# Kernel tuning notes

Hardware: AMD Instinct MI355X
Metric: run time of the kernel (lower is better)

Reference implementation:

```python
import jax, jax.numpy as jnp
import numpy as np

B, S, H, HKV, D = 4, 1024, 32, 8, 128   # batch segments, seq per segment, q heads, kv heads, head dim
N = B * S                                # Ntotal (ragged tokens, equal-length segments)
SCALE = 1.0 / np.sqrt(D)                 # softmax_scale init kwarg
NEG = -1e9


def setup_inputs() -> dict:
    key = jax.random.key(0)
    kq, kk, kv = jax.random.split(key, 3)
    q = jax.random.normal(kq, (N, H, D), jnp.float32)
    k = jax.random.normal(kk, (N, HKV, D), jnp.float32)
    v = jax.random.normal(kv, (N, HKV, D), jnp.float32)
    # RoPE angles, rotate-half convention: concat(freqs, freqs), broadcast over heads
    inv_freq = 1.0 / (10000.0 ** (jnp.arange(D // 2, dtype=jnp.float32) / (D // 2)))
    pos = jnp.arange(S, dtype=jnp.float32)
    ang = pos[:, None] * inv_freq[None, :]                      # [S, D/2]
    idx_theta = jnp.tile(jnp.concatenate([ang, ang], -1), (B, 1))[:, None, :]  # [N,1,D]
    # per-segment causal mask, stacked -> [N, S]
    causal = jnp.where(jnp.arange(S)[None, :] <= jnp.arange(S)[:, None], 0.0, NEG).astype(jnp.float32)
    mask = jnp.tile(causal, (B, 1))
    return {"q": q, "k": k, "v": v, "idx_theta": idx_theta, "mask": mask}


def _rotate_half(x):
    # cat(-x[..., D/2:], x[..., :D/2])
    return jnp.concatenate([-x[..., D // 2:], x[..., : D // 2]], axis=-1)


def reference(q, k, v, idx_theta, mask):
    rep = H // HKV
    # repeat_kv: attention head i uses kv head i // rep (matches torch expand+reshape order)
    kx = jnp.repeat(k, rep, axis=1)                    # [N, H, D]
    vx = jnp.repeat(v, rep, axis=1)
    cos, sin = jnp.cos(idx_theta), jnp.sin(idx_theta)
    qr = q * cos + _rotate_half(q) * sin
    kr = kx * cos + _rotate_half(kx) * sin
    # segment-blocked attention (equal-length segments, vectorized over batch & heads)
    qb = qr.reshape(B, S, H, D)
    kb = kr.reshape(B, S, H, D)
    vb = vx.reshape(B, S, H, D)
    mb = mask.reshape(B, S, S)[:, None, :, :]          # [B,1,S,S]
    scores = jnp.einsum('bqhd,bkhd->bhqk', qb, kb) * SCALE + mb
    l = jax.nn.logsumexp(scores, axis=-1)              # [B,H,S] == max + logsumexp(shifted)
    p = jax.nn.softmax(scores, axis=-1)
    o = jnp.einsum('bhqk,bkhd->bqhd', p, vb)           # [B,S,H,D]
    o = o.reshape(N, H * D)                            # o.reshape(Ntotal, num_head, -1) flattened last two in torch is (N,H,D)->(N,H,D); original reshape(q.shape[0], q.shape[1], -1) keeps [N,H,D]
    o = o.reshape(N, H, D)
    l = l.transpose(0, 2, 1).reshape(N, H, 1)          # [Ntotal, num_head, 1]
    return o, l
```

## Files before the change

kernel.cpp:

```cpp
#include <hip/hip_runtime.h>

#define B_    4
#define S_    1024
#define H_    32
#define HKV_  8
#define D_    128
#define NTOT  (B_*S_)
#define QT_   64
#define KT_   32
#define DPAD  (D_+8)
#define KPAD  (KT_+8)

#define SCALE_ 0.08838834764831845f

typedef __attribute__((ext_vector_type(8))) short bf16x8;
typedef __attribute__((ext_vector_type(4))) short bf16x4;
typedef __attribute__((ext_vector_type(4))) float f32x4;
typedef __attribute__((ext_vector_type(4))) int   int4v;

__device__ __forceinline__ unsigned short f2bf(float f) {
    unsigned int u = __float_as_uint(f);
    u += 0x7FFFu + ((u >> 16) & 1u);
    return (unsigned short)(u >> 16);
}
__device__ __forceinline__ unsigned int pack2bf(float a, float b) {
    return (unsigned int)f2bf(a) | ((unsigned int)f2bf(b) << 16);
}

__global__ void rope_k_kernel(const float* __restrict__ k,
                              const float* __restrict__ theta,
                              unsigned short* __restrict__ kr) {
    int t  = blockIdx.x * blockDim.x + threadIdx.x;
    int g  = t & 7;
    int hk = (t >> 3) & (HKV_ - 1);
    int n  = t >> 6;
    if (n >= NTOT) return;
    int d0 = g * 8;
    const float* kp = k + ((size_t)n * HKV_ + hk) * D_;
    const float* tp = theta + (size_t)n * D_;

    alignas(16) float kl[8], ku[8], thl[8], thu[8];
    *(float4*)&kl[0]  = *(const float4*)(kp + d0);
    *(float4*)&kl[4]  = *(const float4*)(kp + d0 + 4);
    *(float4*)&ku[0]  = *(const float4*)(kp + d0 + 64);
    *(float4*)&ku[4]  = *(const float4*)(kp + d0 + 68);
    *(float4*)&thl[0] = *(const float4*)(tp + d0);
    *(float4*)&thl[4] = *(const float4*)(tp + d0 + 4);
    *(float4*)&thu[0] = *(const float4*)(tp + d0 + 64);
    *(float4*)&thu[4] = *(const float4*)(tp + d0 + 68);

    alignas(16) unsigned short ol[8], ou[8];
#pragma unroll
    for (int j = 0; j < 8; ++j) {
        float sl, cl, su, cu;
        __sincosf(thl[j], &sl, &cl);
        __sincosf(thu[j], &su, &cu);
        ol[j] = f2bf(kl[j] * cl - ku[j] * sl);
        ou[j] = f2bf(ku[j] * cu + kl[j] * su);
    }
    unsigned short* outp = kr + ((size_t)n * HKV_ + hk) * D_;
    *(int4v*)(outp + d0)      = *(const int4v*)ol;
    *(int4v*)(outp + d0 + 64) = *(const int4v*)ou;
}

__global__ void vt_kernel(const float* __restrict__ v,
                          unsigned short* __restrict__ vt) {
    __shared__ unsigned int T[64][64];
    int blk = blockIdx.x;
    int s0  = (blk & (S_/64 - 1)) * 64;
    int hk  = (blk >> 4) & (HKV_ - 1);
    int b   = blk >> 7;
    int tid = threadIdx.x;

#pragma unroll
    for (int i = 0; i < 8; ++i) {
        int u  = tid + 256 * i;
        int s  = u >> 5;
        int G  = u & 31;
        float4 val = *(const float4*)(v + (((size_t)(b * S_ + s0 + s)) * HKV_ + hk) * D_ + G * 4);
        unsigned int* p = &T[s][(G ^ (s & 31)) << 1];
        p[0] = pack2bf(val.x, val.y);
        p[1] = pack2bf(val.z, val.w);
    }
    __syncthreads();
#pragma unroll
    for (int i = 0; i < 4; ++i) {
        int u = tid + 256 * i;
        int d = u >> 3;
        int g = u & 7;
        int G = d >> 2;
        int half = (d >> 1) & 1;
        int hi   = (d & 1) * 16;
        alignas(16) unsigned short tmp[8];
#pragma unroll
        for (int j = 0; j < 8; ++j) {
            int s = g * 8 + j;
            unsigned int w = T[s][(((G ^ (s & 31)) << 1)) + half];
            tmp[j] = (unsigned short)(w >> hi);
        }
        *(int4v*)(vt + (((size_t)(b * HKV_ + hk)) * D_ + d) * S_ + s0 + g * 8) = *(const int4v*)tmp;
    }
}

__global__ __launch_bounds__(256, 4)
void flash_kernel(const float* __restrict__ q,
                  const float* __restrict__ theta,
                  const unsigned short* __restrict__ kr,
                  const unsigned short* __restrict__ vt,
                  float* __restrict__ o_out,
                  float* __restrict__ l_out) {
    __shared__ unsigned short Ks[2][KT_][DPAD];
    __shared__ unsigned short Vs[2][D_][KPAD];

    const int tid  = threadIdx.x;
    const int wave = tid >> 6;
    const int lane = tid & 63;
    const int l16  = lane & 15;
    const int quad = lane >> 4;

    const int bh = blockIdx.x;
    const int b  = bh >> 5;
    const int h  = bh & (H_ - 1);
    const int hk = h >> 2;
    const int qt = (S_/QT_ - 1) - blockIdx.y;
    const int qbase = qt * QT_;
    const int wq   = qbase + wave * 16;
    const int qrow = wq + l16;

    bf16x8 qfrag[4];
    {
        const int n = b * S_ + qrow;
        const float* qp = q + ((size_t)n * H_ + h) * D_;
        const float* tp = theta + (size_t)n * D_;
#pragma unroll
        for (int c = 0; c < 4; ++c) {
            const int d0 = c * 32 + quad * 8;
            const int dp = d0 ^ 64;
            alignas(16) float qa[8], qb[8], th[8];
            *(float4*)&qa[0] = *(const float4*)(qp + d0);
            *(float4*)&qa[4] = *(const float4*)(qp + d0 + 4);
            *(float4*)&qb[0] = *(const float4*)(qp + dp);
            *(float4*)&qb[4] = *(const float4*)(qp + dp + 4);
            *(float4*)&th[0] = *(const float4*)(tp + d0);
            *(float4*)&th[4] = *(const float4*)(tp + d0 + 4);
            alignas(16) unsigned short tmp[8];
#pragma unroll
            for (int j = 0; j < 8; ++j) {
                float sv, cv;
                __sincosf(th[j], &sv, &cv);
                float rot = (d0 < 64) ? -qb[j] : qb[j];
                tmp[j] = f2bf((qa[j] * cv + rot * sv) * SCALE_);
            }
            qfrag[c] = *(const bf16x8*)tmp;
        }
    }

    f32x4 acc[8];
#pragma unroll
    for (int dt = 0; dt < 8; ++dt) acc[dt] = (f32x4){0.f, 0.f, 0.f, 0.f};
    float m_st = -1e30f, l_st = 0.f;

    const unsigned short* kseg = kr + ((size_t)b * S_ * HKV_ + hk) * D_;
    const unsigned short* vseg = vt + ((size_t)(b * HKV_ + hk)) * D_ * S_;

    const int ku0 = tid, ku1 = tid + 256;
    const int kk0 = ku0 >> 4, kg0 = (ku0 & 15) * 8;
    const int kk1 = kk0 + 16,  kg1 = kg0;
    const int vd0 = tid >> 2, vg0 = (tid & 3) * 8;
    const int vd1 = vd0 + 64,  vg1 = vg0;
    int4v pK0, pK1, pV0, pV1;

#define LOAD_TILE(K0)                                                          \
    do {                                                                       \
        pK0 = *(const int4v*)(kseg + (size_t)((K0) + kk0) * (HKV_*D_) + kg0);  \
        pK1 = *(const int4v*)(kseg + (size_t)((K0) + kk1) * (HKV_*D_) + kg1);  \
        pV0 = *(const int4v*)(vseg + (size_t)vd0 * S_ + (K0) + vg0);           \
        pV1 = *(const int4v*)(vseg + (size_t)vd1 * S_ + (K0) + vg1);           \
    } while (0)
#define STORE_TILE(BUF)                                                        \
    do {                                                                       \
        *(int4v*)&Ks[BUF][kk0][kg0] = pK0;                                     \
        *(int4v*)&Ks[BUF][kk1][kg1] = pK1;                                     \
        *(int4v*)&Vs[BUF][vd0][vg0] = pV0;                                     \
        *(int4v*)&Vs[BUF][vd1][vg1] = pV1;                                     \
    } while (0)

    const int n_kt = 2 * (qt + 1);
    LOAD_TILE(0);
    STORE_TILE(0);

    for (int kt = 0; kt < n_kt; ++kt) {
        const int k0 = kt * KT_;
        const int buf = kt & 1;
        __syncthreads();
        if (kt + 1 < n_kt) LOAD_TILE(k0 + KT_);

        int dd = wq + 15 - k0;
        int nact = dd < 0 ? 0 : (dd >> 4) + 1;
        if (nact > 2) nact = 2;

        if (nact > 0) {
            f32x4 sc[2];
#pragma unroll
            for (int kc = 0; kc < 2; ++kc) {
                if (kc < nact) {
                    f32x4 c = (f32x4){0.f, 0.f, 0.f, 0.f};
#pragma unroll
                    for (int cc = 0; cc < 4; ++cc) {
                        bf16x8 kf = *(const bf16x8*)&Ks[buf][kc * 16 + l16][cc * 32 + quad * 8];
                        c = __builtin_amdgcn_mfma_f32_16x16x32_bf16(kf, qfrag[cc], c, 0, 0, 0);
                    }
                    sc[kc] = c;
                }
            }

            float s[8];
#pragma unroll
            for (int kc = 0; kc < 2; ++kc)
#pragma unroll
                for (int r = 0; r < 4; ++r) {
                    int key = k0 + kc * 16 + quad * 4 + r;
                    s[kc * 4 + r] = (kc < nact && key <= qrow) ? sc[kc][r] : -1e30f;
                }
            float tmax = s[0];
#pragma unroll
            for (int i = 1; i < 8; ++i) tmax = fmaxf(tmax, s[i]);
            tmax = fmaxf(tmax, __shfl_xor(tmax, 16));
            tmax = fmaxf(tmax, __shfl_xor(tmax, 32));
            float mnew  = fmaxf(m_st, tmax);
            float alpha = __expf(m_st - mnew);

            unsigned int pk[4];
            float rs = 0.f;
#pragma unroll
            for (int kc = 0; kc < 2; ++kc) {
                float p0 = __expf(s[kc * 4 + 0] - mnew);
                float p1 = __expf(s[kc * 4 + 1] - mnew);
                float p2 = __expf(s[kc * 4 + 2] - mnew);
                float p3 = __expf(s[kc * 4 + 3] - mnew);
                rs += (p0 + p1) + (p2 + p3);
                pk[kc * 2 + 0] = pack2bf(p0, p1);
                pk[kc * 2 + 1] = pack2bf(p2, p3);
            }
            rs += __shfl_xor(rs, 16);
            rs += __shfl_xor(rs, 32);
            l_st = l_st * alpha + rs;
            m_st = mnew;
#pragma unroll
            for (int dt = 0; dt < 8; ++dt) {
                acc[dt][0] *= alpha; acc[dt][1] *= alpha;
                acc[dt][2] *= alpha; acc[dt][3] *= alpha;
            }

#pragma unroll
            for (int kc = 0; kc < 2; ++kc) {
                if (kc < nact) {
                    union { unsigned int u[2]; bf16x4 v; } pb;
                    pb.u[0] = pk[kc * 2 + 0];
                    pb.u[1] = pk[kc * 2 + 1];
#if __has_builtin(__builtin_amdgcn_mfma_f32_16x16x16bf16_1k)
#pragma unroll
                    for (int dt = 0; dt < 8; ++dt) {
                        bf16x4 vf = *(const bf16x4*)&Vs[buf][dt * 16 + l16][kc * 16 + quad * 4];
                        acc[dt] = __builtin_amdgcn_mfma_f32_16x16x16bf16_1k(vf, pb.v, acc[dt], 0, 0, 0);
                    }
#else
                    bf16x8 pb8 = (bf16x8){pb.v[0], pb.v[1], pb.v[2], pb.v[3], 0, 0, 0, 0};
#pragma unroll
                    for (int dt = 0; dt < 8; ++dt) {
                        bf16x4 vf = *(const bf16x4*)&Vs[buf][dt * 16 + l16][kc * 16 + quad * 4];
                        bf16x8 vf8 = (bf16x8){vf[0], vf[1], vf[2], vf[3], 0, 0, 0, 0};
                        acc[dt] = __builtin_amdgcn_mfma_f32_16x16x32_bf16(vf8, pb8, acc[dt], 0, 0, 0);
                    }
#endif
                }
            }
        }

        if (kt + 1 < n_kt) STORE_TILE(1 - buf);
    }

    const float inv = 1.0f / l_st;
    const int n = b * S_ + qrow;
    float* op = o_out + ((size_t)n * H_ + h) * D_;
#pragma unroll
    for (int dt = 0; dt < 8; ++dt) {
        float4 o4 = {acc[dt][0] * inv, acc[dt][1] * inv, acc[dt][2] * inv, acc[dt][3] * inv};
        *(float4*)(op + dt * 16 + quad * 4) = o4;
    }
    if (quad == 0)
        l_out[(size_t)n * H_ + h] = m_st + logf(l_st);
}

extern "C" void kernel_launch(void* const* d_in, const int* in_sizes, int n_in,
                              void* d_out, int out_size, void* d_ws, size_t ws_size,
                              hipStream_t stream) {
    const float* q     = (const float*)d_in[0];
    const float* k     = (const float*)d_in[1];
    const float* v     = (const float*)d_in[2];
    const float* theta = (const float*)d_in[3];

    float* o_out = (float*)d_out;
    float* l_out = o_out + (size_t)NTOT * H_ * D_;

    unsigned short* kr = (unsigned short*)d_ws;
    unsigned short* vt = kr + (size_t)NTOT * HKV_ * D_;

    rope_k_kernel<<<(NTOT * HKV_ * 8) / 256, 256, 0, stream>>>(k, theta, kr);
    vt_kernel<<<B_ * HKV_ * (S_ / 64), 256, 0, stream>>>(v, vt);

    dim3 grid(B_ * H_, S_ / QT_);
    flash_kernel<<<grid, 256, 0, stream>>>(q, theta, kr, vt, o_out, l_out);
}
```

Baseline: 228.2 us.

## Share K/V tiles across GQA heads per block, use exp2 and lazy rescale

Each block now handles one KV head, and its four waves each take one of the four query heads that share it. Every wave processes two 16-row query groups over a 32-row query tile, so each K/V tile loaded into shared memory is reused across the whole GQA group instead of being reloaded per query head. Softmax switches to base-2 exponentials, with log2e folded into the Q scale. The rescale of the running max and accumulators is skipped when no lane's max grows. V padding changes to 36 with split 8-byte stores, and register pressure roughly doubles (two accumulator sets), so launch bounds drop to 3 blocks per CU. The grid shrinks from 128×16 to 32×32 blocks.

```diff
diff --git a/kernel.cpp b/kernel.cpp
--- a/kernel.cpp
+++ b/kernel.cpp
@@ -6,17 +6,20 @@
 #define HKV_  8
 #define D_    128
 #define NTOT  (B_*S_)
-#define QT_   64
+#define QT_   32
 #define KT_   32
 #define DPAD  (D_+8)
-#define KPAD  (KT_+8)
-
-#define SCALE_ 0.08838834764831845f
+#define VPAD  36
+
+#define SCALE_  0.08838834764831845f
+#define LOG2E_  1.4426950408889634f
+#define LN2_    0.6931471805599453f
 
 typedef __attribute__((ext_vector_type(8))) short bf16x8;
 typedef __attribute__((ext_vector_type(4))) short bf16x4;
 typedef __attribute__((ext_vector_type(4))) float f32x4;
 typedef __attribute__((ext_vector_type(4))) int   int4v;
+typedef __attribute__((ext_vector_type(2))) int   int2v;
 
 __device__ __forceinline__ unsigned short f2bf(float f) {
     unsigned int u = __float_as_uint(f);
@@ -102,7 +105,7 @@
     }
 }
 
-__global__ __launch_bounds__(256, 4)
+__global__ __launch_bounds__(256, 3)
 void flash_kernel(const float* __restrict__ q,
                   const float* __restrict__ theta,
                   const unsigned short* __restrict__ kr,
@@ -110,7 +113,7 @@
                   float* __restrict__ o_out,
                   float* __restrict__ l_out) {
     __shared__ unsigned short Ks[2][KT_][DPAD];
-    __shared__ unsigned short Vs[2][D_][KPAD];
+    __shared__ unsigned short Vs[2][D_][VPAD];
 
     const int tid  = threadIdx.x;
     const int wave = tid >> 6;
@@ -118,17 +121,17 @@
     const int l16  = lane & 15;
     const int quad = lane >> 4;
 
-    const int bh = blockIdx.x;
-    const int b  = bh >> 5;
-    const int h  = bh & (H_ - 1);
-    const int hk = h >> 2;
-    const int qt = (S_/QT_ - 1) - blockIdx.y;
+    const int bkv = blockIdx.x;
+    const int b   = bkv >> 3;
+    const int hkv = bkv & 7;
+    const int h   = hkv * 4 + wave;
+    const int qt  = (S_/QT_ - 1) - blockIdx.y;
     const int qbase = qt * QT_;
-    const int wq   = qbase + wave * 16;
-    const int qrow = wq + l16;
-
-    bf16x8 qfrag[4];
-    {
+
+    bf16x8 qfrag[2][4];
+#pragma unroll
+    for (int mg = 0; mg < 2; ++mg) {
+        const int qrow = qbase + mg * 16 + l16;
         const int n = b * S_ + qrow;
         const float* qp = q + ((size_t)n * H_ + h) * D_;
         const float* tp = theta + (size_t)n * D_;
@@ -149,43 +152,47 @@
                 float sv, cv;
                 __sincosf(th[j], &sv, &cv);
                 float rot = (d0 < 64) ? -qb[j] : qb[j];
-                tmp[j] = f2bf((qa[j] * cv + rot * sv) * SCALE_);
-            }
-            qfrag[c] = *(const bf16x8*)tmp;
+                tmp[j] = f2bf((qa[j] * cv + rot * sv) * (SCALE_ * LOG2E_));
+            }
+            qfrag[mg][c] = *(const bf16x8*)tmp;
         }
     }
 
-    f32x4 acc[8];
-#pragma unroll
-    for (int dt = 0; dt < 8; ++dt) acc[dt] = (f32x4){0.f, 0.f, 0.f, 0.f};
-    float m_st = -1e30f, l_st = 0.f;
-
-    const unsigned short* kseg = kr + ((size_t)b * S_ * HKV_ + hk) * D_;
-    const unsigned short* vseg = vt + ((size_t)(b * HKV_ + hk)) * D_ * S_;
-
-    const int ku0 = tid, ku1 = tid + 256;
-    const int kk0 = ku0 >> 4, kg0 = (ku0 & 15) * 8;
-    const int kk1 = kk0 + 16,  kg1 = kg0;
+    f32x4 acc[2][8];
+#pragma unroll
+    for (int mg = 0; mg < 2; ++mg)
+#pragma unroll
+        for (int dt = 0; dt < 8; ++dt) acc[mg][dt] = (f32x4){0.f, 0.f, 0.f, 0.f};
+    float m_st[2] = {-1e30f, -1e30f};
+    float l_st[2] = {0.f, 0.f};
+
+    const unsigned short* kseg = kr + ((size_t)b * S_ * HKV_ + hkv) * D_;
+    const unsigned short* vseg = vt + ((size_t)(b * HKV_ + hkv)) * D_ * S_;
+
+    const int kk0 = tid >> 4, kg0 = (tid & 15) * 8;
+    const int kk1 = kk0 + 16;
     const int vd0 = tid >> 2, vg0 = (tid & 3) * 8;
-    const int vd1 = vd0 + 64,  vg1 = vg0;
+    const int vd1 = vd0 + 64;
     int4v pK0, pK1, pV0, pV1;
 
 #define LOAD_TILE(K0)                                                          \
     do {                                                                       \
         pK0 = *(const int4v*)(kseg + (size_t)((K0) + kk0) * (HKV_*D_) + kg0);  \
-        pK1 = *(const int4v*)(kseg + (size_t)((K0) + kk1) * (HKV_*D_) + kg1);  \
+        pK1 = *(const int4v*)(kseg + (size_t)((K0) + kk1) * (HKV_*D_) + kg0);  \
         pV0 = *(const int4v*)(vseg + (size_t)vd0 * S_ + (K0) + vg0);           \
-        pV1 = *(const int4v*)(vseg + (size_t)vd1 * S_ + (K0) + vg1);           \
+        pV1 = *(const int4v*)(vseg + (size_t)vd1 * S_ + (K0) + vg0);           \
     } while (0)
 #define STORE_TILE(BUF)                                                        \
     do {                                                                       \
         *(int4v*)&Ks[BUF][kk0][kg0] = pK0;                                     \
-        *(int4v*)&Ks[BUF][kk1][kg1] = pK1;                                     \
-        *(int4v*)&Vs[BUF][vd0][vg0] = pV0;                                     \
-        *(int4v*)&Vs[BUF][vd1][vg1] = pV1;                                     \
+        *(int4v*)&Ks[BUF][kk1][kg0] = pK1;                                     \
+        *(int2v*)&Vs[BUF][vd0][vg0]     = (int2v){pV0.x, pV0.y};               \
+        *(int2v*)&Vs[BUF][vd0][vg0 + 4] = (int2v){pV0.z, pV0.w};               \
+        *(int2v*)&Vs[BUF][vd1][vg0]     = (int2v){pV1.x, pV1.y};               \
+        *(int2v*)&Vs[BUF][vd1][vg0 + 4] = (int2v){pV1.z, pV1.w};               \
     } while (0)
 
-    const int n_kt = 2 * (qt + 1);
+    const int n_kt = qt + 1;
     LOAD_TILE(0);
     STORE_TILE(0);
 
@@ -195,11 +202,13 @@
         __syncthreads();
         if (kt + 1 < n_kt) LOAD_TILE(k0 + KT_);
 
-        int dd = wq + 15 - k0;
-        int nact = dd < 0 ? 0 : (dd >> 4) + 1;
-        if (nact > 2) nact = 2;
-
-        if (nact > 0) {
+#pragma unroll
+        for (int mg = 0; mg < 2; ++mg) {
+            const int wq = qbase + mg * 16;
+            const int qrow = wq + l16;
+            int nact = ((wq + 15 - k0) >> 4) + 1;
+            if (nact > 2) nact = 2;
+
             f32x4 sc[2];
 #pragma unroll
             for (int kc = 0; kc < 2; ++kc) {
@@ -208,7 +217,7 @@
 #pragma unroll
                     for (int cc = 0; cc < 4; ++cc) {
                         bf16x8 kf = *(const bf16x8*)&Ks[buf][kc * 16 + l16][cc * 32 + quad * 8];
-                        c = __builtin_amdgcn_mfma_f32_16x16x32_bf16(kf, qfrag[cc], c, 0, 0, 0);
+                        c = __builtin_amdgcn_mfma_f32_16x16x32_bf16(kf, qfrag[mg][cc], c, 0, 0, 0);
                     }
                     sc[kc] = c;
                 }
@@ -227,30 +236,35 @@
             for (int i = 1; i < 8; ++i) tmax = fmaxf(tmax, s[i]);
             tmax = fmaxf(tmax, __shfl_xor(tmax, 16));
             tmax = fmaxf(tmax, __shfl_xor(tmax, 32));
-            float mnew  = fmaxf(m_st, tmax);
-            float alpha = __expf(m_st - mnew);
+
+            if (__any(tmax > m_st[mg])) {
+                float mnew  = fmaxf(m_st[mg], tmax);
+                float alpha = exp2f(m_st[mg] - mnew);
+                l_st[mg] *= alpha;
+                m_st[mg] = mnew;
+#pragma unroll
+                for (int dt = 0; dt < 8; ++dt) {
+                    acc[mg][dt][0] *= alpha; acc[mg][dt][1] *= alpha;
+                    acc[mg][dt][2] *= alpha; acc[mg][dt][3] *= alpha;
+                }
+            }
+            const float mcur = m_st[mg];
 
             unsigned int pk[4];
             float rs = 0.f;
 #pragma unroll
             for (int kc = 0; kc < 2; ++kc) {
-                float p0 = __expf(s[kc * 4 + 0] - mnew);
-                float p1 = __expf(s[kc * 4 + 1] - mnew);
-                float p2 = __expf(s[kc * 4 + 2] - mnew);
-                float p3 = __expf(s[kc * 4 + 3] - mnew);
+                float p0 = exp2f(s[kc * 4 + 0] - mcur);
+                float p1 = exp2f(s[kc * 4 + 1] - mcur);
+                float p2 = exp2f(s[kc * 4 + 2] - mcur);
+                float p3 = exp2f(s[kc * 4 + 3] - mcur);
                 rs += (p0 + p1) + (p2 + p3);
                 pk[kc * 2 + 0] = pack2bf(p0, p1);
                 pk[kc * 2 + 1] = pack2bf(p2, p3);
             }
             rs += __shfl_xor(rs, 16);
             rs += __shfl_xor(rs, 32);
-            l_st = l_st * alpha + rs;
-            m_st = mnew;
-#pragma unroll
-            for (int dt = 0; dt < 8; ++dt) {
-                acc[dt][0] *= alpha; acc[dt][1] *= alpha;
-                acc[dt][2] *= alpha; acc[dt][3] *= alpha;
-            }
+            l_st[mg] += rs;
 
 #pragma unroll
             for (int kc = 0; kc < 2; ++kc) {
@@ -262,7 +276,7 @@
 #pragma unroll
                     for (int dt = 0; dt < 8; ++dt) {
                         bf16x4 vf = *(const bf16x4*)&Vs[buf][dt * 16 + l16][kc * 16 + quad * 4];
-                        acc[dt] = __builtin_amdgcn_mfma_f32_16x16x16bf16_1k(vf, pb.v, acc[dt], 0, 0, 0);
+                        acc[mg][dt] = __builtin_amdgcn_mfma_f32_16x16x16bf16_1k(vf, pb.v, acc[mg][dt], 0, 0, 0);
                     }
 #else
                     bf16x8 pb8 = (bf16x8){pb.v[0], pb.v[1], pb.v[2], pb.v[3], 0, 0, 0, 0};
@@ -270,7 +284,7 @@
                     for (int dt = 0; dt < 8; ++dt) {
                         bf16x4 vf = *(const bf16x4*)&Vs[buf][dt * 16 + l16][kc * 16 + quad * 4];
                         bf16x8 vf8 = (bf16x8){vf[0], vf[1], vf[2], vf[3], 0, 0, 0, 0};
-                        acc[dt] = __builtin_amdgcn_mfma_f32_16x16x32_bf16(vf8, pb8, acc[dt], 0, 0, 0);
+                        acc[mg][dt] = __builtin_amdgcn_mfma_f32_16x16x32_bf16(vf8, pb8, acc[mg][dt], 0, 0, 0);
                     }
 #endif
                 }
@@ -280,16 +294,21 @@
         if (kt + 1 < n_kt) STORE_TILE(1 - buf);
     }
 
-    const float inv = 1.0f / l_st;
-    const int n = b * S_ + qrow;
-    float* op = o_out + ((size_t)n * H_ + h) * D_;
-#pragma unroll
-    for (int dt = 0; dt < 8; ++dt) {
-        float4 o4 = {acc[dt][0] * inv, acc[dt][1] * inv, acc[dt][2] * inv, acc[dt][3] * inv};
-        *(float4*)(op + dt * 16 + quad * 4) = o4;
-    }
-    if (quad == 0)
-        l_out[(size_t)n * H_ + h] = m_st + logf(l_st);
+#pragma unroll
+    for (int mg = 0; mg < 2; ++mg) {
+        const int qrow = qbase + mg * 16 + l16;
+        const float inv = 1.0f / l_st[mg];
+        const int n = b * S_ + qrow;
+        float* op = o_out + ((size_t)n * H_ + h) * D_;
+#pragma unroll
+        for (int dt = 0; dt < 8; ++dt) {
+            float4 o4 = {acc[mg][dt][0] * inv, acc[mg][dt][1] * inv,
+                         acc[mg][dt][2] * inv, acc[mg][dt][3] * inv};
+            *(float4*)(op + dt * 16 + quad * 4) = o4;
+        }
+        if (quad == 0)
+            l_out[(size_t)n * H_ + h] = (m_st[mg] + log2f(l_st[mg])) * LN2_;
+    }
 }
 
 extern "C" void kernel_launch(void* const* d_in, const int* in_sizes, int n_in,
@@ -309,6 +328,6 @@
     rope_k_kernel<<<(NTOT * HKV_ * 8) / 256, 256, 0, stream>>>(k, theta, kr);
     vt_kernel<<<B_ * HKV_ * (S_ / 64), 256, 0, stream>>>(v, vt);
 
-    dim3 grid(B_ * H_, S_ / QT_);
+    dim3 grid(B_ * HKV_, S_ / QT_);
     flash_kernel<<<grid, 256, 0, stream>>>(q, theta, kr, vt, o_out, l_out);
 }
```

New measurement: 235.5 us. +3.2%, slower.
